# Kernel optimization log

Measured on AMD Instinct MI355X. Metric: run time of the kernel, lower is better.

## Reference

```python
import jax, jax.numpy as jnp
from jax import lax
import numpy as np

LAM = 0.95          # config.agent.return_lambda
HORIZON = 333.0     # config.agent.horizon
# slowtar=True, contdisc=False

B, T, D, H = 1024, 16, 5120, 1024


def _mlp(feat, w1, b1, w2, b2, w3, b3):
    # critic MLP -> scalar mean per (b, t); [B,T,D] -> [B,T]
    h = jax.nn.silu(jnp.einsum('btd,dh->bth', feat, w1) + b1)
    h = jax.nn.silu(jnp.einsum('bth,hk->btk', h, w2) + b2)
    return jnp.einsum('bth,h->bt', h, w3) + b3[0]


def setup_inputs() -> dict:
    key = jax.random.key(0)
    ks = jax.random.split(key, 10)
    sc1 = 1.0 / np.sqrt(D)
    sc2 = 1.0 / np.sqrt(H)
    return {
        'feat': jax.random.normal(ks[0], (B, T, D), jnp.float32),
        'rew': jax.random.normal(ks[1], (B, T), jnp.float32),
        'cont': jax.random.uniform(ks[2], (B, T), jnp.float32),
        'net_w1': jax.random.normal(ks[3], (D, H), jnp.float32) * sc1,
        'net_b1': jnp.zeros((H,), jnp.float32),
        'net_w2': jax.random.normal(ks[4], (H, H), jnp.float32) * sc2,
        'net_b2': jnp.zeros((H,), jnp.float32),
        'net_w3': jax.random.normal(ks[5], (H,), jnp.float32) * sc2,
        'net_b3': jnp.zeros((1,), jnp.float32),
        'slow_w1': jax.random.normal(ks[6], (D, H), jnp.float32) * sc1,
        'slow_b1': jnp.zeros((H,), jnp.float32),
        'slow_w2': jax.random.normal(ks[7], (H, H), jnp.float32) * sc2,
        'slow_b2': jnp.zeros((H,), jnp.float32),
        'slow_w3': jax.random.normal(ks[8], (H,), jnp.float32) * sc2,
        'slow_b3': jnp.zeros((1,), jnp.float32),
        'voffset': jax.random.normal(ks[9], (1,), jnp.float32),
        'vscale': jax.random.uniform(jax.random.fold_in(key, 99), (1,), jnp.float32, minval=0.5, maxval=1.5),
    }


def reference(feat, rew, cont, net_w1, net_b1, net_w2, net_b2, net_w3, net_b3,
              slow_w1, slow_b1, slow_w2, slow_b2, slow_w3, slow_b3, voffset, vscale):
    critic = _mlp(feat, net_w1, net_b1, net_w2, net_b2, net_w3, net_b3)        # [B,T]
    slowcritic = _mlp(feat, slow_w1, slow_b1, slow_w2, slow_b2, slow_w3, slow_b3)
    val = critic * vscale[0] + voffset[0]
    slowval = slowcritic * vscale[0] + voffset[0]
    tarval = slowval  # slowtar = True
    discount = 1.0 - 1.0 / HORIZON  # contdisc = False
    disc = cont[:, 1:] * discount                                 # [B,T-1]
    interm = rew[:, 1:] + (1.0 - LAM) * disc * tarval[:, 1:]      # [B,T-1]

    def step(carry, xs):
        i_t, d_t = xs
        r = i_t + d_t * LAM * carry
        return r, r

    # reversed linear recurrence over time: rets[t] = interm[t] + disc[t]*lam*rets[t+1]
    _, ys = lax.scan(step, tarval[:, -1], (interm.T, disc.T), reverse=True)  # [T-1,B]
    ret = ys.T                                                    # [B,T-1]
    return rew, ret, tarval, critic, slowcritic
```

## Files before the change

kernel.cpp:

```cpp
#include <hip/hip_runtime.h>
#include <stdint.h>

typedef unsigned short u16;
typedef __attribute__((ext_vector_type(8))) __bf16 bf16x8;
typedef __attribute__((ext_vector_type(8))) u16 u16x8;
typedef __attribute__((ext_vector_type(4))) u16 u16x4;
typedef __attribute__((ext_vector_type(4))) float f32x4;

#define LAM 0.95f
#define DISCOUNT (1.0f - 1.0f / 333.0f)

constexpr int Bsz = 1024, Tsz = 16, Dsz = 5120, Hsz = 1024;
constexpr int Msz = Bsz * Tsz;
constexpr int Nsz = 2 * Hsz;
constexpr int ES = 136;

__device__ __forceinline__ u16 f2bf(float x) {
  union { float f; uint32_t u; } un; un.f = x;
  uint32_t u = un.u;
  return (u16)((u + 0x7FFFu + ((u >> 16) & 1u)) >> 16);
}
__device__ __forceinline__ void async16(const void* g, void* l) {
  __builtin_amdgcn_global_load_lds(
      (const __attribute__((address_space(1))) uint32_t*)g,
      (__attribute__((address_space(3))) uint32_t*)l, 16, 0, 0);
}

__global__ __launch_bounds__(256) void transpose_cvt(
    const float* __restrict__ src, u16* __restrict__ dst, int K, int N) {
  __shared__ float tile[64][65];
  int k0 = blockIdx.x * 64, n0 = blockIdx.y * 64;
  int tid = threadIdx.x;
#pragma unroll
  for (int i = 0; i < 4; ++i) {
    int idx = i * 256 + tid, rr = idx >> 4, c4 = (idx & 15) * 4;
    float4 v = *(const float4*)&src[(size_t)(k0 + rr) * N + n0 + c4];
    tile[rr][c4 + 0] = v.x; tile[rr][c4 + 1] = v.y;
    tile[rr][c4 + 2] = v.z; tile[rr][c4 + 3] = v.w;
  }
  __syncthreads();
#pragma unroll
  for (int i = 0; i < 4; ++i) {
    int idx = i * 256 + tid, rr = idx >> 4, c4 = (idx & 15) * 4;
    u16x4 o;
    o[0] = f2bf(tile[c4 + 0][rr]); o[1] = f2bf(tile[c4 + 1][rr]);
    o[2] = f2bf(tile[c4 + 2][rr]); o[3] = f2bf(tile[c4 + 3][rr]);
    *(u16x4*)&dst[(size_t)(n0 + rr) * K + k0 + c4] = o;
  }
}

__global__ void prep_small(const float* nb1, const float* sb1, const float* nb2,
                           const float* sb2, const float* nw3, const float* sw3,
                           float* bias1, float* bias2, float* w3cat,
                           float* accN, float* accS) {
  int i = blockIdx.x * 256 + threadIdx.x;
  if (i < 1024) { bias1[i] = nb1[i]; bias2[i] = nb2[i]; w3cat[i] = nw3[i]; }
  else if (i < 2048) { bias1[i] = sb1[i - 1024]; bias2[i] = sb2[i - 1024]; w3cat[i] = sw3[i - 1024]; }
  for (int j = i; j < Msz; j += gridDim.x * 256) { accN[j] = 0.f; accS[j] = 0.f; }
}

__global__ void cvt_f32_to_bf16(const float* __restrict__ src, u16* __restrict__ dst, int n4) {
  int i = blockIdx.x * 256 + threadIdx.x;
  int stride = gridDim.x * 256;
  for (; i < n4; i += stride) {
    float4 v = ((const float4*)src)[i];
    u16x4 o; o[0] = f2bf(v.x); o[1] = f2bf(v.y); o[2] = f2bf(v.z); o[3] = f2bf(v.w);
    ((u16x4*)dst)[i] = o;
  }
}

template <int MODE, bool A_F32>
__global__ __launch_bounds__(256) void gemm_fused(
    const void* __restrict__ Ap, const u16* __restrict__ Bp,
    const float* __restrict__ bias, u16* __restrict__ Out,
    const float* __restrict__ w3cat, float* __restrict__ accN, float* __restrict__ accS,
    int K, int lda, int a_half_off) {
  __shared__ __align__(16) u16 smem[(MODE == 0) ? (128 * ES) : 16384];
  u16* ldsA = smem;
  u16* ldsB = smem + 8192;

  const int tid = threadIdx.x;
  const int lane = tid & 63;
  const int wv = tid >> 6;
  const int wm = (wv >> 1) << 6;
  const int wn = (wv & 1) << 6;
  const int lm = lane & 15, lq = lane >> 4, l7 = lane & 7;

  const int blk = blockIdx.x;
  const int xcd = blk & 7;
  const int l = blk >> 3;
  const int quad = l >> 6;
  const int mi = l & 7, ni = (l >> 3) & 7;
  const int mt = xcd * 16 + ((quad & 1) << 3) + mi;
  const int nt = ((quad >> 1) << 3) + ni;
  const int m0 = mt << 7, n0 = nt << 7;
  const int a_off = (n0 >= Hsz) ? a_half_off : 0;

  const u16* bsrc[4];
  const float* asrcf[4];
  const u16* asrcb[4];
  u16* ldsAd[4];
  u16* ldsBd[4];
#pragma unroll
  for (int i = 0; i < 4; ++i) {
    int cid = i * 256 + tid;
    int row = cid >> 3, ch = cid & 7;
    int kp = ch ^ (row & 7);
    bsrc[i] = Bp + (size_t)(n0 + row) * K + kp * 8;
    if (A_F32) asrcf[i] = (const float*)Ap + (size_t)(m0 + row) * lda + a_off + kp * 8;
    else       asrcb[i] = (const u16*)Ap + (size_t)(m0 + row) * lda + a_off + kp * 8;
    ldsAd[i] = &ldsA[cid * 8];
    ldsBd[i] = &ldsB[cid * 8];
  }

  int rA[4], rB[4];
#pragma unroll
  for (int t = 0; t < 4; ++t) {
    rA[t] = (wm + t * 16 + lm) * 64;
    rB[t] = (wn + t * 16 + lm) * 64;
  }

  f32x4 acc[4][4];
#pragma unroll
  for (int a = 0; a < 4; ++a)
#pragma unroll
    for (int b = 0; b < 4; ++b) acc[a][b] = f32x4{0.f, 0.f, 0.f, 0.f};

  for (int kt = 0; kt < K; kt += 64) {
#pragma unroll
    for (int i = 0; i < 4; ++i) async16(bsrc[i] + kt, ldsBd[i]);
    if (A_F32) {
      float4 v0[4], v1[4];
#pragma unroll
      for (int i = 0; i < 4; ++i) {
        const float* p = asrcf[i] + kt;
        v0[i] = *(const float4*)p;
        v1[i] = *(const float4*)(p + 4);
      }
#pragma unroll
      for (int i = 0; i < 4; ++i) {
        u16x8 pk;
        pk[0] = f2bf(v0[i].x); pk[1] = f2bf(v0[i].y); pk[2] = f2bf(v0[i].z); pk[3] = f2bf(v0[i].w);
        pk[4] = f2bf(v1[i].x); pk[5] = f2bf(v1[i].y); pk[6] = f2bf(v1[i].z); pk[7] = f2bf(v1[i].w);
        *(u16x8*)ldsAd[i] = pk;
      }
    } else {
#pragma unroll
      for (int i = 0; i < 4; ++i) async16(asrcb[i] + kt, ldsAd[i]);
    }
    __syncthreads();
#pragma unroll
    for (int ks = 0; ks < 2; ++ks) {
      const int ck = ((ks << 2) + lq) ^ l7;
      bf16x8 af[4], bfr[4];
#pragma unroll
      for (int t = 0; t < 4; ++t) af[t] = *(const bf16x8*)&ldsA[rA[t] + ck * 8];
#pragma unroll
      for (int t = 0; t < 4; ++t) bfr[t] = *(const bf16x8*)&ldsB[rB[t] + ck * 8];
#pragma unroll
      for (int a = 0; a < 4; ++a)
#pragma unroll
        for (int b = 0; b < 4; ++b)
          acc[a][b] = __builtin_amdgcn_mfma_f32_16x16x32_bf16(bfr[b], af[a], acc[a][b], 0, 0, 0);
    }
    __syncthreads();
  }

  if (MODE == 0) {
#pragma unroll
    for (int a = 0; a < 4; ++a) {
      int ml = wm + a * 16 + lm;
#pragma unroll
      for (int b = 0; b < 4; ++b) {
        int nb = wn + b * 16 + lq * 4;
        u16x4 pk;
#pragma unroll
        for (int rr = 0; rr < 4; ++rr) {
          float v = acc[a][b][rr] + bias[n0 + nb + rr];
          v = v * (1.0f / (1.0f + __expf(-v)));
          pk[rr] = f2bf(v);
        }
        *(u16x4*)&smem[ml * ES + nb] = pk;
      }
    }
    __syncthreads();
#pragma unroll
    for (int i = 0; i < 8; ++i) {
      int r = i * 16 + (tid >> 4);
      int c = (tid & 15) * 8;
      u16x8 vv = *(const u16x8*)&smem[r * ES + c];
      *(u16x8*)&Out[(size_t)(m0 + r) * Nsz + n0 + c] = vv;
    }
  } else {
    float pr[4] = {0.f, 0.f, 0.f, 0.f};
#pragma unroll
    for (int a = 0; a < 4; ++a) {
#pragma unroll
      for (int b = 0; b < 4; ++b) {
        int nb = n0 + wn + b * 16 + lq * 4;
#pragma unroll
        for (int rr = 0; rr < 4; ++rr) {
          float v = acc[a][b][rr] + bias[nb + rr];
          v = v * (1.0f / (1.0f + __expf(-v)));
          pr[a] += v * w3cat[nb + rr];
        }
      }
    }
    float* accp = (n0 < Hsz) ? accN : accS;
#pragma unroll
    for (int a = 0; a < 4; ++a) {
      pr[a] += __shfl_xor(pr[a], 16);
      pr[a] += __shfl_xor(pr[a], 32);
      if (lq == 0) atomicAdd(&accp[m0 + wm + a * 16 + lm], pr[a]);
    }
  }
}

__global__ void finalize_scan(const float* __restrict__ accN, const float* __restrict__ accS,
                              const float* __restrict__ nb3, const float* __restrict__ sb3,
                              const float* __restrict__ voff, const float* __restrict__ vscl,
                              const float* __restrict__ rew, const float* __restrict__ cont,
                              float* __restrict__ o_rew, float* __restrict__ o_ret,
                              float* __restrict__ o_tar, float* __restrict__ o_cri,
                              float* __restrict__ o_slo) {
  __shared__ float star[Tsz], srew[Tsz], scont[Tsz];
  int b = blockIdx.x;
  int t = threadIdx.x;
  if (t < Tsz) {
    int m = b * Tsz + t;
    float c = accN[m] + nb3[0];
    float s = accS[m] + sb3[0];
    float tv = s * vscl[0] + voff[0];
    o_cri[m] = c; o_slo[m] = s; o_tar[m] = tv;
    float rw = rew[m];
    o_rew[m] = rw;
    star[t] = tv; srew[t] = rw; scont[t] = cont[m];
  }
  __syncthreads();
  if (t == 0) {
    float carry = star[Tsz - 1];
    for (int k = Tsz - 2; k >= 0; --k) {
      float d = scont[k + 1] * DISCOUNT;
      carry = srew[k + 1] + (1.0f - LAM) * d * star[k + 1] + d * LAM * carry;
      o_ret[b * (Tsz - 1) + k] = carry;
    }
  }
}

constexpr size_t WT1_OFF = 0;
constexpr size_t WT1_BYTES = (size_t)Nsz * Dsz * 2;
constexpr size_t WT2_OFF = WT1_OFF + WT1_BYTES;
constexpr size_t WT2_BYTES = (size_t)Nsz * Hsz * 2;
constexpr size_t B1_OFF = WT2_OFF + WT2_BYTES;
constexpr size_t B2_OFF = B1_OFF + 8192;
constexpr size_t W3_OFF = B2_OFF + 8192;
constexpr size_t ACCN_OFF = W3_OFF + 8192;
constexpr size_t ACCS_OFF = ACCN_OFF + (size_t)Msz * 4;
constexpr size_t H1_OFF = ACCS_OFF + (size_t)Msz * 4;
constexpr size_t H_BYTES = (size_t)Msz * Nsz * 2;
constexpr size_t FEATB_OFF = H1_OFF + H_BYTES;
constexpr size_t FEATB_BYTES = (size_t)Msz * Dsz * 2;
constexpr size_t NEED_BIG = FEATB_OFF + FEATB_BYTES;

extern "C" void kernel_launch(void* const* d_in, const int* in_sizes, int n_in,
                              void* d_out, int out_size, void* d_ws, size_t ws_size,
                              hipStream_t stream) {
  const float* feat = (const float*)d_in[0];
  const float* rew  = (const float*)d_in[1];
  const float* cont = (const float*)d_in[2];
  const float* nw1  = (const float*)d_in[3];
  const float* nb1  = (const float*)d_in[4];
  const float* nw2  = (const float*)d_in[5];
  const float* nb2  = (const float*)d_in[6];
  const float* nw3  = (const float*)d_in[7];
  const float* nb3  = (const float*)d_in[8];
  const float* sw1  = (const float*)d_in[9];
  const float* sb1  = (const float*)d_in[10];
  const float* sw2  = (const float*)d_in[11];
  const float* sb2  = (const float*)d_in[12];
  const float* sw3  = (const float*)d_in[13];
  const float* sb3  = (const float*)d_in[14];
  const float* voff = (const float*)d_in[15];
  const float* vscl = (const float*)d_in[16];

  char* ws = (char*)d_ws;
  u16* wt1 = (u16*)(ws + WT1_OFF);
  u16* wt2 = (u16*)(ws + WT2_OFF);
  float* bias1 = (float*)(ws + B1_OFF);
  float* bias2 = (float*)(ws + B2_OFF);
  float* w3cat = (float*)(ws + W3_OFF);
  float* accN = (float*)(ws + ACCN_OFF);
  float* accS = (float*)(ws + ACCS_OFF);
  u16* h1 = (u16*)(ws + H1_OFF);
  u16* featb = (u16*)(ws + FEATB_OFF);
  const bool big = ws_size >= NEED_BIG;

  float* out = (float*)d_out;
  float* o_rew = out;
  float* o_ret = out + 16384;
  float* o_tar = out + 31744;
  float* o_cri = out + 48128;
  float* o_slo = out + 64512;

  transpose_cvt<<<dim3(Dsz / 64, Hsz / 64), 256, 0, stream>>>(nw1, wt1, Dsz, Hsz);
  transpose_cvt<<<dim3(Dsz / 64, Hsz / 64), 256, 0, stream>>>(sw1, wt1 + (size_t)Hsz * Dsz, Dsz, Hsz);
  transpose_cvt<<<dim3(Hsz / 64, Hsz / 64), 256, 0, stream>>>(nw2, wt2, Hsz, Hsz);
  transpose_cvt<<<dim3(Hsz / 64, Hsz / 64), 256, 0, stream>>>(sw2, wt2 + (size_t)Hsz * Hsz, Hsz, Hsz);
  prep_small<<<8, 256, 0, stream>>>(nb1, sb1, nb2, sb2, nw3, sw3, bias1, bias2, w3cat, accN, accS);

  const int gemm_grid = (Msz / 128) * (Nsz / 128);
  if (big) {
    cvt_f32_to_bf16<<<4096, 256, 0, stream>>>(feat, featb, Msz * Dsz / 4);
    gemm_fused<0, false><<<gemm_grid, 256, 0, stream>>>(
        featb, wt1, bias1, h1, nullptr, nullptr, nullptr, Dsz, Dsz, 0);
  } else {
    gemm_fused<0, true><<<gemm_grid, 256, 0, stream>>>(
        feat, wt1, bias1, h1, nullptr, nullptr, nullptr, Dsz, Dsz, 0);
  }
  gemm_fused<1, false><<<gemm_grid, 256, 0, stream>>>(
      h1, wt2, bias2, nullptr, w3cat, accN, accS, Hsz, Nsz, Hsz);
  finalize_scan<<<Bsz, 64, 0, stream>>>(accN, accS, nb3, sb3, voff, vscl, rew, cont,
                                        o_rew, o_ret, o_tar, o_cri, o_slo);
}
```

Measured before the change: 1.043 ms.

## Merge prep kernels, widen bf16 conversion, and specialize layer-2 GEMM with BK=128

Merges the four weight transpose-convert launches and the small bias/accumulator init into one prep_all kernel, which removes several launches and tail gaps. The feature conversion now handles 8 floats per thread with 16-byte stores. The layer-2 GEMM becomes its own kernel with a 128-wide K tile (64 KB LDS, a 16-way XOR swizzle), halving the number of K iterations and barriers. The larger LDS footprint may reduce occupancy. Zeroing of accS relies on accS sitting directly after accN in the workspace.

Result: faster. 1.019 ms (-2.3%).

```diff
diff --git a/kernel.cpp b/kernel.cpp
--- a/kernel.cpp
+++ b/kernel.cpp
@@ -26,56 +26,66 @@
       (__attribute__((address_space(3))) uint32_t*)l, 16, 0, 0);
 }
 
-__global__ __launch_bounds__(256) void transpose_cvt(
-    const float* __restrict__ src, u16* __restrict__ dst, int K, int N) {
-  __shared__ float tile[64][65];
-  int k0 = blockIdx.x * 64, n0 = blockIdx.y * 64;
-  int tid = threadIdx.x;
-#pragma unroll
-  for (int i = 0; i < 4; ++i) {
-    int idx = i * 256 + tid, rr = idx >> 4, c4 = (idx & 15) * 4;
-    float4 v = *(const float4*)&src[(size_t)(k0 + rr) * N + n0 + c4];
-    tile[rr][c4 + 0] = v.x; tile[rr][c4 + 1] = v.y;
-    tile[rr][c4 + 2] = v.z; tile[rr][c4 + 3] = v.w;
-  }
-  __syncthreads();
-#pragma unroll
-  for (int i = 0; i < 4; ++i) {
-    int idx = i * 256 + tid, rr = idx >> 4, c4 = (idx & 15) * 4;
-    u16x4 o;
-    o[0] = f2bf(tile[c4 + 0][rr]); o[1] = f2bf(tile[c4 + 1][rr]);
-    o[2] = f2bf(tile[c4 + 2][rr]); o[3] = f2bf(tile[c4 + 3][rr]);
-    *(u16x4*)&dst[(size_t)(n0 + rr) * K + k0 + c4] = o;
-  }
-}
-
-__global__ void prep_small(const float* nb1, const float* sb1, const float* nb2,
-                           const float* sb2, const float* nw3, const float* sw3,
-                           float* bias1, float* bias2, float* w3cat,
-                           float* accN, float* accS) {
-  int i = blockIdx.x * 256 + threadIdx.x;
-  if (i < 1024) { bias1[i] = nb1[i]; bias2[i] = nb2[i]; w3cat[i] = nw3[i]; }
-  else if (i < 2048) { bias1[i] = sb1[i - 1024]; bias2[i] = sb2[i - 1024]; w3cat[i] = sw3[i - 1024]; }
-  for (int j = i; j < Msz; j += gridDim.x * 256) { accN[j] = 0.f; accS[j] = 0.f; }
-}
-
-__global__ void cvt_f32_to_bf16(const float* __restrict__ src, u16* __restrict__ dst, int n4) {
+__global__ __launch_bounds__(256) void prep_all(
+    const float* __restrict__ nw1, const float* __restrict__ sw1,
+    const float* __restrict__ nw2, const float* __restrict__ sw2,
+    const float* nb1, const float* sb1, const float* nb2, const float* sb2,
+    const float* nw3, const float* sw3,
+    u16* __restrict__ wt1, u16* __restrict__ wt2,
+    float* bias1, float* bias2, float* w3cat, float* accs) {
+  const int blk = blockIdx.x;
+  const int tid = threadIdx.x;
+  if (blk < 3072) {
+    const float* src; u16* dst; int K, t;
+    if (blk < 1280)      { src = nw1; dst = wt1;                        K = Dsz; t = blk; }
+    else if (blk < 2560) { src = sw1; dst = wt1 + (size_t)Hsz * Dsz;    K = Dsz; t = blk - 1280; }
+    else if (blk < 2816) { src = nw2; dst = wt2;                        K = Hsz; t = blk - 2560; }
+    else                 { src = sw2; dst = wt2 + (size_t)Hsz * Hsz;    K = Hsz; t = blk - 2816; }
+    const int ktiles = K / 64;
+    const int k0 = (t % ktiles) * 64, n0 = (t / ktiles) * 64;
+    __shared__ float tile[64][65];
+#pragma unroll
+    for (int i = 0; i < 4; ++i) {
+      int idx = i * 256 + tid, rr = idx >> 4, c4 = (idx & 15) * 4;
+      float4 v = *(const float4*)&src[(size_t)(k0 + rr) * Hsz + n0 + c4];
+      tile[rr][c4 + 0] = v.x; tile[rr][c4 + 1] = v.y;
+      tile[rr][c4 + 2] = v.z; tile[rr][c4 + 3] = v.w;
+    }
+    __syncthreads();
+#pragma unroll
+    for (int i = 0; i < 4; ++i) {
+      int idx = i * 256 + tid, rr = idx >> 4, c4 = (idx & 15) * 4;
+      u16x4 o;
+      o[0] = f2bf(tile[c4 + 0][rr]); o[1] = f2bf(tile[c4 + 1][rr]);
+      o[2] = f2bf(tile[c4 + 2][rr]); o[3] = f2bf(tile[c4 + 3][rr]);
+      *(u16x4*)&dst[(size_t)(n0 + rr) * K + k0 + c4] = o;
+    }
+  } else {
+    int i = (blk - 3072) * 256 + tid;
+    if (i < 1024) { bias1[i] = nb1[i]; bias2[i] = nb2[i]; w3cat[i] = nw3[i]; }
+    else if (i < 2048) { bias1[i] = sb1[i - 1024]; bias2[i] = sb2[i - 1024]; w3cat[i] = sw3[i - 1024]; }
+    for (int j = i; j < 2 * Msz; j += 40 * 256) accs[j] = 0.f;
+  }
+}
+
+__global__ void cvt_f32_to_bf16(const float* __restrict__ src, u16* __restrict__ dst, int n8) {
   int i = blockIdx.x * 256 + threadIdx.x;
   int stride = gridDim.x * 256;
-  for (; i < n4; i += stride) {
-    float4 v = ((const float4*)src)[i];
-    u16x4 o; o[0] = f2bf(v.x); o[1] = f2bf(v.y); o[2] = f2bf(v.z); o[3] = f2bf(v.w);
-    ((u16x4*)dst)[i] = o;
-  }
-}
-
-template <int MODE, bool A_F32>
-__global__ __launch_bounds__(256) void gemm_fused(
+  for (; i < n8; i += stride) {
+    float4 v0 = ((const float4*)src)[2 * i];
+    float4 v1 = ((const float4*)src)[2 * i + 1];
+    u16x8 o;
+    o[0] = f2bf(v0.x); o[1] = f2bf(v0.y); o[2] = f2bf(v0.z); o[3] = f2bf(v0.w);
+    o[4] = f2bf(v1.x); o[5] = f2bf(v1.y); o[6] = f2bf(v1.z); o[7] = f2bf(v1.w);
+    ((u16x8*)dst)[i] = o;
+  }
+}
+
+template <bool A_F32>
+__global__ __launch_bounds__(256) void gemm1_k(
     const void* __restrict__ Ap, const u16* __restrict__ Bp,
-    const float* __restrict__ bias, u16* __restrict__ Out,
-    const float* __restrict__ w3cat, float* __restrict__ accN, float* __restrict__ accS,
-    int K, int lda, int a_half_off) {
-  __shared__ __align__(16) u16 smem[(MODE == 0) ? (128 * ES) : 16384];
+    const float* __restrict__ bias, u16* __restrict__ Out, int K) {
+  __shared__ __align__(16) u16 smem[128 * ES];
   u16* ldsA = smem;
   u16* ldsB = smem + 8192;
 
@@ -94,7 +104,6 @@
   const int mt = xcd * 16 + ((quad & 1) << 3) + mi;
   const int nt = ((quad >> 1) << 3) + ni;
   const int m0 = mt << 7, n0 = nt << 7;
-  const int a_off = (n0 >= Hsz) ? a_half_off : 0;
 
   const u16* bsrc[4];
   const float* asrcf[4];
@@ -107,8 +116,8 @@
     int row = cid >> 3, ch = cid & 7;
     int kp = ch ^ (row & 7);
     bsrc[i] = Bp + (size_t)(n0 + row) * K + kp * 8;
-    if (A_F32) asrcf[i] = (const float*)Ap + (size_t)(m0 + row) * lda + a_off + kp * 8;
-    else       asrcb[i] = (const u16*)Ap + (size_t)(m0 + row) * lda + a_off + kp * 8;
+    if (A_F32) asrcf[i] = (const float*)Ap + (size_t)(m0 + row) * K + kp * 8;
+    else       asrcb[i] = (const u16*)Ap + (size_t)(m0 + row) * K + kp * 8;
     ldsAd[i] = &ldsA[cid * 8];
     ldsBd[i] = &ldsB[cid * 8];
   }
@@ -166,53 +175,118 @@
     __syncthreads();
   }
 
-  if (MODE == 0) {
-#pragma unroll
-    for (int a = 0; a < 4; ++a) {
-      int ml = wm + a * 16 + lm;
-#pragma unroll
-      for (int b = 0; b < 4; ++b) {
-        int nb = wn + b * 16 + lq * 4;
-        u16x4 pk;
-#pragma unroll
-        for (int rr = 0; rr < 4; ++rr) {
-          float v = acc[a][b][rr] + bias[n0 + nb + rr];
-          v = v * (1.0f / (1.0f + __expf(-v)));
-          pk[rr] = f2bf(v);
-        }
-        *(u16x4*)&smem[ml * ES + nb] = pk;
+#pragma unroll
+  for (int a = 0; a < 4; ++a) {
+    int ml = wm + a * 16 + lm;
+#pragma unroll
+    for (int b = 0; b < 4; ++b) {
+      int nb = wn + b * 16 + lq * 4;
+      u16x4 pk;
+#pragma unroll
+      for (int rr = 0; rr < 4; ++rr) {
+        float v = acc[a][b][rr] + bias[n0 + nb + rr];
+        v = v * (1.0f / (1.0f + __expf(-v)));
+        pk[rr] = f2bf(v);
       }
-    }
-    __syncthreads();
-#pragma unroll
-    for (int i = 0; i < 8; ++i) {
-      int r = i * 16 + (tid >> 4);
-      int c = (tid & 15) * 8;
-      u16x8 vv = *(const u16x8*)&smem[r * ES + c];
-      *(u16x8*)&Out[(size_t)(m0 + r) * Nsz + n0 + c] = vv;
-    }
-  } else {
-    float pr[4] = {0.f, 0.f, 0.f, 0.f};
-#pragma unroll
-    for (int a = 0; a < 4; ++a) {
-#pragma unroll
-      for (int b = 0; b < 4; ++b) {
-        int nb = n0 + wn + b * 16 + lq * 4;
-#pragma unroll
-        for (int rr = 0; rr < 4; ++rr) {
-          float v = acc[a][b][rr] + bias[nb + rr];
-          v = v * (1.0f / (1.0f + __expf(-v)));
-          pr[a] += v * w3cat[nb + rr];
-        }
+      *(u16x4*)&smem[ml * ES + nb] = pk;
+    }
+  }
+  __syncthreads();
+#pragma unroll
+  for (int i = 0; i < 8; ++i) {
+    int r = i * 16 + (tid >> 4);
+    int c = (tid & 15) * 8;
+    u16x8 vv = *(const u16x8*)&smem[r * ES + c];
+    *(u16x8*)&Out[(size_t)(m0 + r) * Nsz + n0 + c] = vv;
+  }
+}
+
+__global__ __launch_bounds__(256) void gemm2_k(
+    const u16* __restrict__ Ap, const u16* __restrict__ Bp,
+    const float* __restrict__ bias, const float* __restrict__ w3cat,
+    float* __restrict__ accN, float* __restrict__ accS) {
+  __shared__ __align__(16) u16 ldsA[128 * 128];
+  __shared__ __align__(16) u16 ldsB[128 * 128];
+
+  const int tid = threadIdx.x;
+  const int lane = tid & 63;
+  const int wv = tid >> 6;
+  const int wm = (wv >> 1) << 6;
+  const int wn = (wv & 1) << 6;
+  const int lm = lane & 15, lq = lane >> 4;
+
+  const int blk = blockIdx.x;
+  const int xcd = blk & 7;
+  const int l = blk >> 3;
+  const int quad = l >> 6;
+  const int mi = l & 7, ni = (l >> 3) & 7;
+  const int mt = xcd * 16 + ((quad & 1) << 3) + mi;
+  const int nt = ((quad >> 1) << 3) + ni;
+  const int m0 = mt << 7, n0 = nt << 7;
+  const int a_off = (n0 >= Hsz) ? Hsz : 0;
+
+  uint32_t aoff[8], boff[8];
+  u16 *ldsAd[8], *ldsBd[8];
+#pragma unroll
+  for (int i = 0; i < 8; ++i) {
+    int cid = i * 256 + tid;
+    int row = cid >> 4, ch = cid & 15;
+    int kp = ch ^ (row & 15);
+    aoff[i] = (uint32_t)(m0 + row) * Nsz + a_off + kp * 8;
+    boff[i] = (uint32_t)(n0 + row) * Hsz + kp * 8;
+    ldsAd[i] = &ldsA[cid * 8];
+    ldsBd[i] = &ldsB[cid * 8];
+  }
+
+  f32x4 acc[4][4];
+#pragma unroll
+  for (int a = 0; a < 4; ++a)
+#pragma unroll
+    for (int b = 0; b < 4; ++b) acc[a][b] = f32x4{0.f, 0.f, 0.f, 0.f};
+
+  for (int kt = 0; kt < Hsz; kt += 128) {
+#pragma unroll
+    for (int i = 0; i < 8; ++i) async16(Bp + boff[i] + kt, ldsBd[i]);
+#pragma unroll
+    for (int i = 0; i < 8; ++i) async16(Ap + aoff[i] + kt, ldsAd[i]);
+    __syncthreads();
+#pragma unroll
+    for (int ks = 0; ks < 4; ++ks) {
+      const int ck = ((ks << 2) + lq) ^ lm;
+      bf16x8 af[4], bfr[4];
+#pragma unroll
+      for (int t = 0; t < 4; ++t) af[t] = *(const bf16x8*)&ldsA[(wm + t * 16 + lm) * 128 + ck * 8];
+#pragma unroll
+      for (int t = 0; t < 4; ++t) bfr[t] = *(const bf16x8*)&ldsB[(wn + t * 16 + lm) * 128 + ck * 8];
+#pragma unroll
+      for (int a = 0; a < 4; ++a)
+#pragma unroll
+        for (int b = 0; b < 4; ++b)
+          acc[a][b] = __builtin_amdgcn_mfma_f32_16x16x32_bf16(bfr[b], af[a], acc[a][b], 0, 0, 0);
+    }
+    __syncthreads();
+  }
+
+  float pr[4] = {0.f, 0.f, 0.f, 0.f};
+#pragma unroll
+  for (int a = 0; a < 4; ++a) {
+#pragma unroll
+    for (int b = 0; b < 4; ++b) {
+      int nb = n0 + wn + b * 16 + lq * 4;
+#pragma unroll
+      for (int rr = 0; rr < 4; ++rr) {
+        float v = acc[a][b][rr] + bias[nb + rr];
+        v = v * (1.0f / (1.0f + __expf(-v)));
+        pr[a] += v * w3cat[nb + rr];
       }
     }
-    float* accp = (n0 < Hsz) ? accN : accS;
-#pragma unroll
-    for (int a = 0; a < 4; ++a) {
-      pr[a] += __shfl_xor(pr[a], 16);
-      pr[a] += __shfl_xor(pr[a], 32);
-      if (lq == 0) atomicAdd(&accp[m0 + wm + a * 16 + lm], pr[a]);
-    }
+  }
+  float* accp = (n0 < Hsz) ? accN : accS;
+#pragma unroll
+  for (int a = 0; a < 4; ++a) {
+    pr[a] += __shfl_xor(pr[a], 16);
+    pr[a] += __shfl_xor(pr[a], 32);
+    if (lq == 0) atomicAdd(&accp[m0 + wm + a * 16 + lm], pr[a]);
   }
 }
 
@@ -302,23 +376,17 @@
   float* o_cri = out + 48128;
   float* o_slo = out + 64512;
 
-  transpose_cvt<<<dim3(Dsz / 64, Hsz / 64), 256, 0, stream>>>(nw1, wt1, Dsz, Hsz);
-  transpose_cvt<<<dim3(Dsz / 64, Hsz / 64), 256, 0, stream>>>(sw1, wt1 + (size_t)Hsz * Dsz, Dsz, Hsz);
-  transpose_cvt<<<dim3(Hsz / 64, Hsz / 64), 256, 0, stream>>>(nw2, wt2, Hsz, Hsz);
-  transpose_cvt<<<dim3(Hsz / 64, Hsz / 64), 256, 0, stream>>>(sw2, wt2 + (size_t)Hsz * Hsz, Hsz, Hsz);
-  prep_small<<<8, 256, 0, stream>>>(nb1, sb1, nb2, sb2, nw3, sw3, bias1, bias2, w3cat, accN, accS);
+  prep_all<<<3112, 256, 0, stream>>>(nw1, sw1, nw2, sw2, nb1, sb1, nb2, sb2, nw3, sw3,
+                                     wt1, wt2, bias1, bias2, w3cat, accN);
 
   const int gemm_grid = (Msz / 128) * (Nsz / 128);
   if (big) {
-    cvt_f32_to_bf16<<<4096, 256, 0, stream>>>(feat, featb, Msz * Dsz / 4);
-    gemm_fused<0, false><<<gemm_grid, 256, 0, stream>>>(
-        featb, wt1, bias1, h1, nullptr, nullptr, nullptr, Dsz, Dsz, 0);
+    cvt_f32_to_bf16<<<4096, 256, 0, stream>>>(feat, featb, Msz * Dsz / 8);
+    gemm1_k<false><<<gemm_grid, 256, 0, stream>>>(featb, wt1, bias1, h1, Dsz);
   } else {
-    gemm_fused<0, true><<<gemm_grid, 256, 0, stream>>>(
-        feat, wt1, bias1, h1, nullptr, nullptr, nullptr, Dsz, Dsz, 0);
-  }
-  gemm_fused<1, false><<<gemm_grid, 256, 0, stream>>>(
-      h1, wt2, bias2, nullptr, w3cat, accN, accS, Hsz, Nsz, Hsz);
+    gemm1_k<true><<<gemm_grid, 256, 0, stream>>>(feat, wt1, bias1, h1, Dsz);
+  }
+  gemm2_k<<<gemm_grid, 256, 0, stream>>>(h1, wt2, bias2, w3cat, accN, accS);
   finalize_scan<<<Bsz, 64, 0, stream>>>(accN, accS, nb3, sb3, voff, vscl, rew, cont,
                                         o_rew, o_ret, o_tar, o_cri, o_slo);
 }
```
